# Optimization experiments

Hardware: AMD Instinct MI355X
Metric: run time of the kernel (lower is better)

The kernel has to match this reference:

```python
import jax, jax.numpy as jnp
import numpy as np

N_HEAD = 16
D = 1024
LV = 2048
HEAD_DIM = D // N_HEAD
B = 2
LQ = 2048
LN_EPS = 1e-5


def setup_inputs() -> dict:
    key = jax.random.key(0)
    ks = jax.random.split(key, 8)
    s = 0.02
    v = jax.random.normal(ks[0], (B, LV, D), dtype=jnp.float32)
    q = jax.random.normal(ks[1], (B, LQ, D), dtype=jnp.float32)
    # per-head attn linear: d -> lv
    Wa = jax.random.normal(ks[2], (N_HEAD, D, LV), dtype=jnp.float32) * s
    ba = jnp.zeros((N_HEAD, LV), dtype=jnp.float32)
    # per-head layernorm over d
    gamma = jnp.ones((N_HEAD, D), dtype=jnp.float32)
    beta = jnp.zeros((N_HEAD, D), dtype=jnp.float32)
    # per-head proj (FilteredLinear modeled as affine): d -> head_dim
    Wp = jax.random.normal(ks[3], (N_HEAD, D, HEAD_DIM), dtype=jnp.float32) * s
    bp = jnp.zeros((N_HEAD, HEAD_DIM), dtype=jnp.float32)
    return {"v": v, "q": q, "Wa": Wa, "ba": ba, "gamma": gamma,
            "beta": beta, "Wp": Wp, "bp": bp}


def _mha(v, q, Wa, ba, gamma, beta, Wp, bp):
    # attn: [H, B, Lq, Lv] = relu(q @ Wa_h + ba_h)  (batched across heads)
    attn = jax.nn.relu(jnp.einsum('bqd,hdl->hbql', q, Wa)
                       + ba[:, None, None, :])
    # external-attention aggregation: [H, B, Lq, D]
    agg = jnp.einsum('hbql,bld->hbqd', attn, v)
    # per-head LayerNorm over last dim (d)
    mu = jnp.mean(agg, axis=-1, keepdims=True)
    var = jnp.var(agg, axis=-1, keepdims=True)
    normed = (agg - mu) * jax.lax.rsqrt(var + LN_EPS)
    normed = normed * gamma[:, None, None, :] + beta[:, None, None, :]
    # per-head projection to head_dim: [H, B, Lq, head_dim]
    heads = jnp.einsum('hbqd,hde->hbqe', normed, Wp) + bp[:, None, None, :]
    # concat heads along feature dim -> [B, Lq, D]
    return heads.transpose(1, 2, 0, 3).reshape(q.shape[0], q.shape[1], -1)


def reference(v, q, Wa, ba, gamma, beta, Wp, bp):
    return _mha(v, q, Wa, ba, gamma, beta, Wp, bp)
```

## Files before the change

### kernel.cpp

```cpp
#include <hip/hip_runtime.h>
#include <hip/hip_bf16.h>

typedef __attribute__((ext_vector_type(8))) short short8;
typedef __attribute__((ext_vector_type(4))) float f32x4;

#define N_HEAD 16
#define DMODEL 1024
#define LV 2048
#define LQ 2048
#define BATCH 2
#define HEAD_DIM 64

template <int N> struct IC { static constexpr int v = N; };

__device__ inline ushort f2bf(float f) {
    union { float f; unsigned u; } v; v.f = f;
    unsigned r = v.u + 0x7fffu + ((v.u >> 16) & 1u);
    return (ushort)(r >> 16);
}
__device__ inline float bf2f(ushort h) {
    union { unsigned u; float f; } v; v.u = ((unsigned)h) << 16;
    return v.f;
}

__global__ __launch_bounds__(256) void cast_bf16(const float* __restrict__ src,
                                                 ushort* __restrict__ dst, int n) {
    int i = (blockIdx.x * 256 + threadIdx.x) * 4;
    if (i < n) {
        float4 v = *(const float4*)(src + i);
        ushort4 o;
        o.x = f2bf(v.x); o.y = f2bf(v.y); o.z = f2bf(v.z); o.w = f2bf(v.w);
        *(ushort4*)(dst + i) = o;
    }
}

__global__ __launch_bounds__(256) void transpose_cast(const float* __restrict__ src,
                                                      ushort* __restrict__ dst,
                                                      int R, int C) {
    __shared__ float t[32][33];
    size_t zoff = (size_t)blockIdx.z * R * C;
    int c0 = blockIdx.x * 32, r0 = blockIdx.y * 32;
    int tx = threadIdx.x, ty = threadIdx.y;
#pragma unroll
    for (int i = 0; i < 4; ++i)
        t[ty + i * 8][tx] = src[zoff + (size_t)(r0 + ty + i * 8) * C + c0 + tx];
    __syncthreads();
#pragma unroll
    for (int i = 0; i < 4; ++i)
        dst[zoff + (size_t)(c0 + ty + i * 8) * R + r0 + tx] = f2bf(t[tx][ty + i * 8]);
}

template <bool RELU>
__global__ __launch_bounds__(512, 2) void gemm256(
    const ushort* __restrict__ A, const ushort* __restrict__ B,
    ushort* __restrict__ Cout, const float* __restrict__ bias,
    int K,
    long sA_b, long sA_h, long sB_b, long sB_h, long sC_z, int ldc, long sBias_h)
{
    __shared__ __align__(16) char smem[131072];

    const int z = blockIdx.z, b = z & 1, h = z >> 1;
    A += (size_t)b * sA_b + (size_t)h * sA_h;
    B += (size_t)b * sB_b + (size_t)h * sB_h;
    const float* biasp = bias ? bias + (size_t)h * sBias_h : nullptr;

    const int bm0 = blockIdx.y * 256;
    const int bn0 = blockIdx.x * 256;
    const int T = threadIdx.x;
    const int lane = T & 63, wid = T >> 6;
    const int wr = wid >> 2, wc = wid & 3;
    const int fr = lane & 15, fq = lane >> 4;
    const int laneoff = fr * 64 + ((fq * 16) ^ ((fr >> 3) << 5));

    const int s_fr  = (T >> 2) & 15;
    const int s_csw = ((T & 3) * 16) ^ ((s_fr >> 3) << 5);
    const int s_rh  = ((T >> 6) << 4) + s_fr;
    const ushort* gA = A + (size_t)(bm0 + s_rh) * K + (s_csw >> 1);
    const ushort* gB = B + (size_t)(bn0 + s_rh) * K + (s_csw >> 1);
    char* smc = smem;

    const int nt = K >> 5;

    auto stage = [&](int op, int half, int kt) {
        const ushort* src = (op ? gB : gA) + ((size_t)half * 128) * K + (size_t)kt * 32;
        char* dst = smc + (((kt & 3) * 2 + op) << 14) + (half << 13) + (T << 4);
        __builtin_amdgcn_global_load_lds(
            (const __attribute__((address_space(1))) void*)src,
            (__attribute__((address_space(3))) void*)dst, 16, 0, 0);
    };

    f32x4 acc[8][4];
#pragma unroll
    for (int m = 0; m < 8; ++m)
#pragma unroll
        for (int n = 0; n < 4; ++n)
#pragma unroll
            for (int j = 0; j < 4; ++j) acc[m][n][j] = 0.f;

#pragma unroll
    for (int tt = 0; tt < 3; ++tt) {
        stage(0, 0, tt); stage(0, 1, tt);
        stage(1, 0, tt); stage(1, 1, tt);
    }
    asm volatile("s_waitcnt vmcnt(8)" ::: "memory");
    asm volatile("s_barrier" ::: "memory");

    auto tile = [&](int t, auto DS, auto VM) {
        constexpr int do_stage = decltype(DS)::v;
        constexpr int vm = decltype(VM)::v;
        const char* sA = smc + (((t & 3) * 2 + 0) << 14) + wr * 8192 + laneoff;
        const char* sB = smc + (((t & 3) * 2 + 1) << 14) + wc * 4096 + laneoff;
        short8 a[8], bfr[4];

#pragma unroll
        for (int m = 0; m < 4; ++m) a[m] = *(const short8*)(sA + m * 1024);
#pragma unroll
        for (int n = 0; n < 4; ++n) bfr[n] = *(const short8*)(sB + n * 1024);
        if constexpr (do_stage) { stage(0, 0, t + 3); stage(0, 1, t + 3); }
        asm volatile("s_barrier" ::: "memory");
        __builtin_amdgcn_sched_barrier(0);
        __builtin_amdgcn_s_setprio(1);
#pragma unroll
        for (int m = 0; m < 4; ++m)
#pragma unroll
            for (int n = 0; n < 4; ++n)
                acc[m][n] = __builtin_amdgcn_mfma_f32_16x16x32_bf16(
                    a[m], bfr[n], acc[m][n], 0, 0, 0);
        __builtin_amdgcn_s_setprio(0);
        __builtin_amdgcn_sched_barrier(0);
        asm volatile("s_barrier" ::: "memory");

#pragma unroll
        for (int m = 4; m < 8; ++m) a[m] = *(const short8*)(sA + m * 1024);
        if constexpr (do_stage) { stage(1, 0, t + 3); stage(1, 1, t + 3); }
        if constexpr (vm == 8)      asm volatile("s_waitcnt vmcnt(8)" ::: "memory");
        else if constexpr (vm == 4) asm volatile("s_waitcnt vmcnt(4)" ::: "memory");
        else if constexpr (vm == 0) asm volatile("s_waitcnt vmcnt(0)" ::: "memory");
        asm volatile("s_barrier" ::: "memory");
        __builtin_amdgcn_sched_barrier(0);
        __builtin_amdgcn_s_setprio(1);
#pragma unroll
        for (int m = 4; m < 8; ++m)
#pragma unroll
            for (int n = 0; n < 4; ++n)
                acc[m][n] = __builtin_amdgcn_mfma_f32_16x16x32_bf16(
                    a[m], bfr[n], acc[m][n], 0, 0, 0);
        __builtin_amdgcn_s_setprio(0);
        __builtin_amdgcn_sched_barrier(0);
        asm volatile("s_barrier" ::: "memory");
    };

    for (int t = 0; t < nt - 3; ++t) tile(t, IC<1>{}, IC<8>{});
    tile(nt - 3, IC<0>{}, IC<4>{});
    tile(nt - 2, IC<0>{}, IC<0>{});
    tile(nt - 1, IC<0>{}, IC<-1>{});

    ushort* C = Cout + (size_t)z * sC_z;
    const int row0 = bm0 + wr * 128;
    const int col0 = bn0 + wc * 64;
#pragma unroll
    for (int n = 0; n < 4; ++n) {
        const int c = col0 + n * 16 + fr;
        const float bvv = biasp ? biasp[c] : 0.f;
#pragma unroll
        for (int m = 0; m < 8; ++m) {
            const int r = row0 + m * 16 + fq * 4;
#pragma unroll
            for (int j = 0; j < 4; ++j) {
                float val = acc[m][n][j] + bvv;
                if (RELU) val = fmaxf(val, 0.f);
                C[(size_t)(r + j) * ldc + c] = f2bf(val);
            }
        }
    }
}

__global__ __launch_bounds__(256) void ln_kernel(ushort* __restrict__ agg,
                                                 const float* __restrict__ gamma,
                                                 const float* __restrict__ beta) {
    const int wid = threadIdx.x >> 6, lane = threadIdx.x & 63;
    const size_t row = (size_t)blockIdx.x * 4 + wid;
    const int h = (int)(row >> 12);
    ushort* p = agg + row * 1024 + lane * 16;
    short8 r0 = *(const short8*)p;
    short8 r1 = *(const short8*)(p + 8);
    float x[16];
#pragma unroll
    for (int j = 0; j < 8; ++j) { x[j] = bf2f((ushort)r0[j]); x[8 + j] = bf2f((ushort)r1[j]); }
    float s = 0.f, s2 = 0.f;
#pragma unroll
    for (int j = 0; j < 16; ++j) { s += x[j]; s2 += x[j] * x[j]; }
    for (int o = 1; o < 64; o <<= 1) {
        s  += __shfl_xor(s,  o, 64);
        s2 += __shfl_xor(s2, o, 64);
    }
    float mu  = s * (1.0f / 1024.0f);
    float var = s2 * (1.0f / 1024.0f) - mu * mu;
    float rs  = rsqrtf(fmaxf(var, 0.f) + 1e-5f);
    const float* g  = gamma + (size_t)h * 1024 + lane * 16;
    const float* bt = beta  + (size_t)h * 1024 + lane * 16;
    short8 o0, o1;
#pragma unroll
    for (int j = 0; j < 8; ++j) {
        o0[j] = (short)f2bf((x[j]     - mu) * rs * g[j]     + bt[j]);
        o1[j] = (short)f2bf((x[8 + j] - mu) * rs * g[8 + j] + bt[8 + j]);
    }
    *(short8*)p = o0;
    *(short8*)(p + 8) = o1;
}

__global__ __launch_bounds__(256) void proj_kernel(const ushort* __restrict__ normed,
                                                   const ushort* __restrict__ WpT,
                                                   const float* __restrict__ bp,
                                                   float* __restrict__ out,
                                                   int h_base) {
    const int z = blockIdx.y, b = z & 1, h = z >> 1;
    const int hg = h_base + h;
    const int wid = threadIdx.x >> 6, lane = threadIdx.x & 63;
    const int fr = lane & 15, fq = lane >> 4;
    const int m0 = (blockIdx.x * 4 + wid) * 16;

    const ushort* Abase = normed + ((size_t)z * 2048 + m0 + fr) * 1024 + fq * 8;
    const ushort* Bbase = WpT + (size_t)hg * 64 * 1024 + (size_t)fr * 1024 + fq * 8;

    f32x4 acc[4];
#pragma unroll
    for (int n = 0; n < 4; ++n)
#pragma unroll
        for (int j = 0; j < 4; ++j) acc[n][j] = 0.f;

    for (int kt = 0; kt < 32; ++kt) {
        short8 a = *(const short8*)(Abase + kt * 32);
#pragma unroll
        for (int n = 0; n < 4; ++n) {
            short8 bb = *(const short8*)(Bbase + n * 16 * 1024 + kt * 32);
            acc[n] = __builtin_amdgcn_mfma_f32_16x16x32_bf16(a, bb, acc[n], 0, 0, 0);
        }
    }
#pragma unroll
    for (int n = 0; n < 4; ++n) {
        int c = hg * 64 + n * 16 + fr;
        float bvv = bp[hg * 64 + n * 16 + fr];
#pragma unroll
        for (int j = 0; j < 4; ++j)
            out[(size_t)b * 2048 * 1024 + (size_t)(m0 + fq * 4 + j) * 1024 + c] =
                acc[n][j] + bvv;
    }
}

extern "C" void kernel_launch(void* const* d_in, const int* in_sizes, int n_in,
                              void* d_out, int out_size, void* d_ws, size_t ws_size,
                              hipStream_t stream) {
    const float* v     = (const float*)d_in[0];
    const float* q     = (const float*)d_in[1];
    const float* Wa    = (const float*)d_in[2];
    const float* ba    = (const float*)d_in[3];
    const float* gamma = (const float*)d_in[4];
    const float* beta  = (const float*)d_in[5];
    const float* Wp    = (const float*)d_in[6];
    const float* bp    = (const float*)d_in[7];
    float* out = (float*)d_out;

    const size_t MB = 1ull << 20;
    char* ws = (char*)d_ws;
    ushort* qbf = (ushort*)(ws);
    ushort* vT  = (ushort*)(ws + 8 * MB);
    ushort* WpT = (ushort*)(ws + 16 * MB);
    int NH = 1;
    {
        const int cands[5] = {16, 8, 4, 2, 1};
        for (int i = 0; i < 5; ++i) {
            if ((size_t)(18 + 28 * cands[i]) * MB <= ws_size) { NH = cands[i]; break; }
        }
    }
    ushort* WaT_c  = (ushort*)(ws + 18 * MB);
    ushort* attn_c = (ushort*)(ws + (18 + (size_t)4 * NH) * MB);
    ushort* agg_c  = (ushort*)(ws + (18 + (size_t)20 * NH) * MB);

    dim3 tb(32, 8);
    cast_bf16<<<4096, 256, 0, stream>>>(q, qbf, BATCH * LQ * DMODEL);
    transpose_cast<<<dim3(DMODEL / 32, LV / 32, BATCH), tb, 0, stream>>>(v, vT, LV, DMODEL);
    transpose_cast<<<dim3(HEAD_DIM / 32, DMODEL / 32, N_HEAD), tb, 0, stream>>>(Wp, WpT, DMODEL, HEAD_DIM);

    for (int h0 = 0; h0 < N_HEAD; h0 += NH) {
        transpose_cast<<<dim3(LV / 32, DMODEL / 32, NH), tb, 0, stream>>>(
            Wa + (size_t)h0 * DMODEL * LV, WaT_c, DMODEL, LV);

        gemm256<true><<<dim3(LV / 256, LQ / 256, NH * 2), 512, 0, stream>>>(
            qbf, WaT_c, attn_c, ba + (size_t)h0 * LV, DMODEL,
            (long)LQ * DMODEL, 0L,
            0L, (long)LV * DMODEL,
            (long)LQ * LV, LV, (long)LV);

        gemm256<false><<<dim3(DMODEL / 256, LQ / 256, NH * 2), 512, 0, stream>>>(
            attn_c, vT, agg_c, nullptr, LV,
            (long)LQ * LV, (long)2 * LQ * LV,
            (long)DMODEL * LV, 0L,
            (long)LQ * DMODEL, DMODEL, 0L);

        ln_kernel<<<(NH * 2 * LQ) / 4, 256, 0, stream>>>(
            agg_c, gamma + (size_t)h0 * DMODEL, beta + (size_t)h0 * DMODEL);

        proj_kernel<<<dim3(LQ / 64, NH * 2), 256, 0, stream>>>(
            agg_c, WpT, bp, out, h0);
    }
}
```

Before: 831.0 us.

## Double-buffer LDS fragments in registers and collapse GEMM main loop to one barrier

Restructures the bf16 GEMM main loop so each step loads the next tile's LDS fragments into a second register set while running all 32 MFMAs on the current set. Staging of all four global->LDS loads for tile t+3 is issued at once, and the two half-tile phases with four barriers per tile become one phase with a single barrier plus lgkmcnt/vmcnt waits. The goal is to overlap LDS reads with MFMA and cut barrier overhead, at the cost of doubled fragment registers (possible occupancy/spill pressure) and subtler ring-buffer hazard timing across the 4-slot LDS buffer.

```diff
diff --git a/kernel.cpp b/kernel.cpp
--- a/kernel.cpp
+++ b/kernel.cpp
@@ -88,72 +88,68 @@
             (const __attribute__((address_space(1))) void*)src,
             (__attribute__((address_space(3))) void*)dst, 16, 0, 0);
     };
-
-    f32x4 acc[8][4];
-#pragma unroll
-    for (int m = 0; m < 8; ++m)
-#pragma unroll
-        for (int n = 0; n < 4; ++n)
-#pragma unroll
-            for (int j = 0; j < 4; ++j) acc[m][n][j] = 0.f;
-
-#pragma unroll
-    for (int tt = 0; tt < 3; ++tt) {
-        stage(0, 0, tt); stage(0, 1, tt);
-        stage(1, 0, tt); stage(1, 1, tt);
-    }
-    asm volatile("s_waitcnt vmcnt(8)" ::: "memory");
-    asm volatile("s_barrier" ::: "memory");
-
-    auto tile = [&](int t, auto DS, auto VM) {
-        constexpr int do_stage = decltype(DS)::v;
-        constexpr int vm = decltype(VM)::v;
+    auto stage4 = [&](int kt) {
+        stage(0, 0, kt); stage(0, 1, kt); stage(1, 0, kt); stage(1, 1, kt);
+    };
+
+    struct Frags { short8 a[8]; short8 bb[4]; };
+    auto ldfrag = [&](int t, Frags& F) {
         const char* sA = smc + (((t & 3) * 2 + 0) << 14) + wr * 8192 + laneoff;
         const char* sB = smc + (((t & 3) * 2 + 1) << 14) + wc * 4096 + laneoff;
-        short8 a[8], bfr[4];
-
-#pragma unroll
-        for (int m = 0; m < 4; ++m) a[m] = *(const short8*)(sA + m * 1024);
-#pragma unroll
-        for (int n = 0; n < 4; ++n) bfr[n] = *(const short8*)(sB + n * 1024);
-        if constexpr (do_stage) { stage(0, 0, t + 3); stage(0, 1, t + 3); }
-        asm volatile("s_barrier" ::: "memory");
-        __builtin_amdgcn_sched_barrier(0);
+#pragma unroll
+        for (int m = 0; m < 8; ++m) F.a[m] = *(const short8*)(sA + m * 1024);
+#pragma unroll
+        for (int n = 0; n < 4; ++n) F.bb[n] = *(const short8*)(sB + n * 1024);
+    };
+
+    f32x4 acc[8][4];
+#pragma unroll
+    for (int m = 0; m < 8; ++m)
+#pragma unroll
+        for (int n = 0; n < 4; ++n)
+#pragma unroll
+            for (int j = 0; j < 4; ++j) acc[m][n][j] = 0.f;
+
+    auto mfma32 = [&](Frags& F) {
         __builtin_amdgcn_s_setprio(1);
 #pragma unroll
-        for (int m = 0; m < 4; ++m)
+        for (int m = 0; m < 8; ++m)
 #pragma unroll
             for (int n = 0; n < 4; ++n)
                 acc[m][n] = __builtin_amdgcn_mfma_f32_16x16x32_bf16(
-                    a[m], bfr[n], acc[m][n], 0, 0, 0);
+                    F.a[m], F.bb[n], acc[m][n], 0, 0, 0);
         __builtin_amdgcn_s_setprio(0);
+    };
+
+    auto step = [&](int t, Frags& rd, Frags& mm, auto VM, auto DOSTAGE, auto DOREAD) {
+        constexpr int vm = decltype(VM)::v;
+        if constexpr (decltype(DOREAD)::v)  ldfrag(t + 1, rd);
+        if constexpr (decltype(DOSTAGE)::v) stage4(t + 3);
+        mfma32(mm);
         __builtin_amdgcn_sched_barrier(0);
+        if constexpr (vm == 4)
+            asm volatile("s_waitcnt vmcnt(4) lgkmcnt(12)" ::: "memory");
+        else if constexpr (vm == 0)
+            asm volatile("s_waitcnt vmcnt(0) lgkmcnt(12)" ::: "memory");
+        else
+            asm volatile("s_waitcnt lgkmcnt(12)" ::: "memory");
         asm volatile("s_barrier" ::: "memory");
-
-#pragma unroll
-        for (int m = 4; m < 8; ++m) a[m] = *(const short8*)(sA + m * 1024);
-        if constexpr (do_stage) { stage(1, 0, t + 3); stage(1, 1, t + 3); }
-        if constexpr (vm == 8)      asm volatile("s_waitcnt vmcnt(8)" ::: "memory");
-        else if constexpr (vm == 4) asm volatile("s_waitcnt vmcnt(4)" ::: "memory");
-        else if constexpr (vm == 0) asm volatile("s_waitcnt vmcnt(0)" ::: "memory");
-        asm volatile("s_barrier" ::: "memory");
-        __builtin_amdgcn_sched_barrier(0);
-        __builtin_amdgcn_s_setprio(1);
-#pragma unroll
-        for (int m = 4; m < 8; ++m)
-#pragma unroll
-            for (int n = 0; n < 4; ++n)
-                acc[m][n] = __builtin_amdgcn_mfma_f32_16x16x32_bf16(
-                    a[m], bfr[n], acc[m][n], 0, 0, 0);
-        __builtin_amdgcn_s_setprio(0);
-        __builtin_amdgcn_sched_barrier(0);
-        asm volatile("s_barrier" ::: "memory");
-    };
-
-    for (int t = 0; t < nt - 3; ++t) tile(t, IC<1>{}, IC<8>{});
-    tile(nt - 3, IC<0>{}, IC<4>{});
-    tile(nt - 2, IC<0>{}, IC<0>{});
-    tile(nt - 1, IC<0>{}, IC<-1>{});
+    };
+
+    stage4(0); stage4(1); stage4(2);
+    asm volatile("s_waitcnt vmcnt(4)" ::: "memory");
+    asm volatile("s_barrier" ::: "memory");
+    Frags fA, fB;
+    ldfrag(0, fA);
+
+    for (int t = 0; t < nt - 4; t += 2) {
+        step(t,     fB, fA, IC<4>{}, IC<1>{}, IC<1>{});
+        step(t + 1, fA, fB, IC<4>{}, IC<1>{}, IC<1>{});
+    }
+    step(nt - 4, fB, fA, IC<4>{},  IC<1>{}, IC<1>{});
+    step(nt - 3, fA, fB, IC<0>{},  IC<0>{}, IC<1>{});
+    step(nt - 2, fB, fA, IC<-1>{}, IC<0>{}, IC<1>{});
+    step(nt - 1, fA, fB, IC<-1>{}, IC<0>{}, IC<0>{});
 
     ushort* C = Cout + (size_t)z * sC_z;
     const int row0 = bm0 + wr * 128;
```

Result: no change. 831.3 us (+0.0%).
